# Kernel optimization log

Hardware: AMD Instinct MI355X
Metric: run time of the kernel (lower is better)

The kernel has to match this reference:

```python
import jax, jax.numpy as jnp
import numpy as np

HEIGHT, WIDTH = 480, 640
IN_CHANNEL, OUT_CHANNEL, FILTER = 6, 32, 3
B, N = 8, 16384
X_COL, Y_COL, P_COL = 1, 2, 3


def setup_inputs() -> dict:
    key = jax.random.key(0)
    k1, k2, k3, k4 = jax.random.split(key, 4)
    xytp = jax.random.uniform(k1, (B, N, 4), dtype=jnp.float32)
    features = jax.random.normal(k2, (B, N, IN_CHANNEL), dtype=jnp.float32)
    fan_in = FILTER * FILTER * (IN_CHANNEL + 2)
    W = jax.random.normal(k3, (FILTER, FILTER, IN_CHANNEL + 2, OUT_CHANNEL), dtype=jnp.float32) / jnp.sqrt(jnp.float32(fan_in))
    bias = jax.random.normal(k4, (OUT_CHANNEL,), dtype=jnp.float32) * 0.05
    return {"xytp": xytp, "features": features, "W": W, "bias": bias}


def reference(xytp, features, W, bias):
    Bc, Nc = xytp.shape[:2]
    # polarity channels: [pos, neg] concatenated with extra features -> Cin = in_channel + 2
    p = xytp[..., P_COL:P_COL + 1]
    feat = jnp.concatenate([p, 1.0 - p, features], axis=-1)  # [B, N, Cin]
    # event2image: round normalized coords to integer pixel grid (values in [0, H] / [0, W])
    yy = jnp.round(xytp[..., Y_COL] * HEIGHT).astype(jnp.int32)  # [B, N]
    xx = jnp.round(xytp[..., X_COL] * WIDTH).astype(jnp.int32)   # [B, N]
    H1, W1 = HEIGHT + 1, WIDTH + 1
    Cin = feat.shape[-1]
    bidx = jnp.broadcast_to(jnp.arange(Bc)[:, None], (Bc, Nc))
    # scn.InputLayer(mode=3): sum features at duplicate coordinates -> dense scatter-add
    grid = jnp.zeros((Bc, H1, W1, Cin), feat.dtype).at[bidx, yy, xx].add(feat)
    # SubmanifoldConvolution: inactive sites hold zero features, so a dense SAME conv
    # computes the identical gather+GEMM+scatter result at every active site.
    out_grid = jax.lax.conv_general_dilated(
        grid, W, window_strides=(1, 1), padding='SAME',
        dimension_numbers=('NHWC', 'HWIO', 'NHWC')) + bias
    # scn.OutputLayer: each input event reads the feature at its (b, y, x) site
    return out_grid[bidx, yy, xx]  # [B, N, out_channel]
```

## Files before the change

kernel.cpp:

```cpp
#include <hip/hip_runtime.h>
#include <hip/hip_bf16.h>

#define HEIGHT 480
#define WIDTH  640
#define IN_CH  6
#define CIN    8
#define COUT   32
#define BATCH  8
#define NPTS   16384
#define NPTOT  (BATCH * NPTS)
#define GH 483
#define GW 643
#define NCELLS ((size_t)BATCH * GH * GW)
#define NWORDS 77644

__device__ __forceinline__ size_t cell_idx(int b, int gy, int gx) {
    return ((size_t)b * GH + gy) * GW + gx;
}

__device__ __forceinline__ void point_cell(const float4 q, int point,
                                           int& b, int& gy, int& gx) {
    gy = (int)rintf(q.z * (float)HEIGHT) + 1;
    gx = (int)rintf(q.y * (float)WIDTH) + 1;
    b  = point >> 14;
}

__global__ void zero_masks_kernel(uint4* __restrict__ m4, int n4) {
    int i = blockIdx.x * blockDim.x + threadIdx.x;
    if (i < n4) m4[i] = make_uint4(0u, 0u, 0u, 0u);
}

__global__ void count_kernel(const float4* __restrict__ xytp,
                             unsigned int* __restrict__ occ,
                             unsigned int* __restrict__ multi) {
    int point = blockIdx.x * blockDim.x + threadIdx.x;
    if (point >= NPTOT) return;
    float4 q = xytp[point];
    int b, gy, gx;
    point_cell(q, point, b, gy, gx);
    size_t ci = cell_idx(b, gy, gx);
    unsigned int word = (unsigned int)(ci >> 5);
    unsigned int bit  = 1u << (ci & 31);
    unsigned int old = atomicOr(&occ[word], bit);
    if (old & bit) atomicOr(&multi[word], bit);
}

__global__ void prep_kernel(const unsigned int* __restrict__ multi,
                            float* __restrict__ grid) {
    int w = blockIdx.x * blockDim.x + threadIdx.x;
    if (w >= NWORDS) return;
    unsigned int m = multi[w];
    const float4 z = make_float4(0.f, 0.f, 0.f, 0.f);
    while (m) {
        int bpos = __ffs(m) - 1;
        m &= m - 1;
        size_t ci = ((size_t)w << 5) + bpos;
        float* cell = grid + (ci << 3);
        *(float4*)(cell)     = z;
        *(float4*)(cell + 4) = z;
    }
}

__global__ void write_kernel(const float4* __restrict__ xytp,
                             const float*  __restrict__ feats,
                             const unsigned int* __restrict__ multi,
                             float* __restrict__ grid) {
    int point = blockIdx.x * blockDim.x + threadIdx.x;
    if (point >= NPTOT) return;
    float4 q = xytp[point];
    int b, gy, gx;
    point_cell(q, point, b, gy, gx);
    size_t ci = cell_idx(b, gy, gx);

    const float* f = feats + (size_t)point * IN_CH;
    float v0 = q.w, v1 = 1.0f - q.w;
    float f0 = f[0], f1 = f[1], f2 = f[2], f3 = f[3], f4 = f[4], f5 = f[5];

    unsigned int word = (unsigned int)(ci >> 5);
    unsigned int bit  = 1u << (ci & 31);

    float* cell = grid + (ci << 3);
    if (!(multi[word] & bit)) {
        *(float4*)(cell)     = make_float4(v0, v1, f0, f1);
        *(float4*)(cell + 4) = make_float4(f2, f3, f4, f5);
    } else {
        unsafeAtomicAdd(cell + 0, v0);
        unsafeAtomicAdd(cell + 1, v1);
        unsafeAtomicAdd(cell + 2, f0);
        unsafeAtomicAdd(cell + 3, f1);
        unsafeAtomicAdd(cell + 4, f2);
        unsafeAtomicAdd(cell + 5, f3);
        unsafeAtomicAdd(cell + 6, f4);
        unsafeAtomicAdd(cell + 7, f5);
    }
}

__global__ void conv_gather_kernel(const float4* __restrict__ xytp,
                                   const float*  __restrict__ grid,
                                   const unsigned int* __restrict__ occ,
                                   const float*  __restrict__ W,
                                   const float*  __restrict__ bias,
                                   float* __restrict__ out) {
    int idx = blockIdx.x * blockDim.x + threadIdx.x;
    if (idx >= NPTOT) return;
    float4 q = xytp[idx];
    int b, gy, gx;
    point_cell(q, idx, b, gy, gx);
    size_t base_ci = cell_idx(b, gy - 1, gx - 1);

    float acc[COUT];
#pragma unroll
    for (int c = 0; c < COUT; ++c) acc[c] = bias[c];

#pragma unroll
    for (int ky = 0; ky < 3; ++ky) {
        size_t ci_row = base_ci + (size_t)ky * GW;
        size_t word = ci_row >> 5;
        int sh = (int)(ci_row & 31);
        unsigned int w0 = occ[word];
        unsigned int w1 = occ[word + 1];
        unsigned int bits = (unsigned int)(((((unsigned long long)w1) << 32) | w0) >> sh) & 7u;
#pragma unroll
        for (int kx = 0; kx < 3; ++kx) {
            if (bits & (1u << kx)) {
                size_t ci = ci_row + kx;
                const float* cell = grid + (ci << 3);
                float4 g0 = *(const float4*)(cell);
                float4 g1 = *(const float4*)(cell + 4);
                float gv[CIN] = {g0.x, g0.y, g0.z, g0.w, g1.x, g1.y, g1.z, g1.w};
                const float* wp = W + (ky * 3 + kx) * CIN * COUT;
#pragma unroll
                for (int ci2 = 0; ci2 < CIN; ++ci2) {
#pragma unroll
                    for (int c = 0; c < COUT; ++c) {
                        acc[c] = fmaf(gv[ci2], wp[ci2 * COUT + c], acc[c]);
                    }
                }
            }
        }
    }

    float* o = out + (size_t)idx * COUT;
#pragma unroll
    for (int c = 0; c < COUT; c += 4) {
        *(float4*)(o + c) = make_float4(acc[c], acc[c + 1], acc[c + 2], acc[c + 3]);
    }
}

extern "C" void kernel_launch(void* const* d_in, const int* in_sizes, int n_in,
                              void* d_out, int out_size, void* d_ws, size_t ws_size,
                              hipStream_t stream) {
    const float4* xytp  = (const float4*)d_in[0];
    const float*  feats = (const float*)d_in[1];
    const float*  W     = (const float*)d_in[2];
    const float*  bias  = (const float*)d_in[3];
    float* out = (float*)d_out;

    float* grid = (float*)d_ws;
    const size_t grid_bytes = NCELLS * CIN * sizeof(float);
    unsigned int* occ   = (unsigned int*)((char*)d_ws + grid_bytes);
    unsigned int* multi = occ + NWORDS;
    (void)ws_size;

    const int blk = 256;
    const int nblk_pts = (NPTOT + blk - 1) / blk;

    const int n4 = (2 * NWORDS) / 4;
    zero_masks_kernel<<<(n4 + blk - 1) / blk, blk, 0, stream>>>((uint4*)occ, n4);

    count_kernel<<<nblk_pts, blk, 0, stream>>>(xytp, occ, multi);

    prep_kernel<<<(NWORDS + blk - 1) / blk, blk, 0, stream>>>(multi, grid);

    write_kernel<<<nblk_pts, blk, 0, stream>>>(xytp, feats, multi, grid);

    conv_gather_kernel<<<nblk_pts, blk, 0, stream>>>(xytp, grid, occ, W, bias, out);
}
```

Before: 44.97 us.

## Merge prep into count kernel and split conv gather across output halves

Drops the separate prep kernel: count_kernel now zeroes a cell itself when it sees a duplicate hit, which saves one launch. The conv gather kernel runs two threads per point, each computing 16 output channels, to double parallelism and cut accumulator registers. All 9 neighbour loads are issued up front without branches (an unoccupied neighbour loads the centre cell and is masked to zero), so loads can overlap instead of being serialised by divergent branches. The cost is that grid loads and occupancy-bit work are duplicated across the two halves, and the masked FMAs are always executed.

```diff
diff --git a/kernel.cpp b/kernel.cpp
--- a/kernel.cpp
+++ b/kernel.cpp
@@ -32,7 +32,8 @@
 
 __global__ void count_kernel(const float4* __restrict__ xytp,
                              unsigned int* __restrict__ occ,
-                             unsigned int* __restrict__ multi) {
+                             unsigned int* __restrict__ multi,
+                             float* __restrict__ grid) {
     int point = blockIdx.x * blockDim.x + threadIdx.x;
     if (point >= NPTOT) return;
     float4 q = xytp[point];
@@ -42,20 +43,10 @@
     unsigned int word = (unsigned int)(ci >> 5);
     unsigned int bit  = 1u << (ci & 31);
     unsigned int old = atomicOr(&occ[word], bit);
-    if (old & bit) atomicOr(&multi[word], bit);
-}
-
-__global__ void prep_kernel(const unsigned int* __restrict__ multi,
-                            float* __restrict__ grid) {
-    int w = blockIdx.x * blockDim.x + threadIdx.x;
-    if (w >= NWORDS) return;
-    unsigned int m = multi[w];
-    const float4 z = make_float4(0.f, 0.f, 0.f, 0.f);
-    while (m) {
-        int bpos = __ffs(m) - 1;
-        m &= m - 1;
-        size_t ci = ((size_t)w << 5) + bpos;
+    if (old & bit) {
+        atomicOr(&multi[word], bit);
         float* cell = grid + (ci << 3);
+        const float4 z = make_float4(0.f, 0.f, 0.f, 0.f);
         *(float4*)(cell)     = z;
         *(float4*)(cell + 4) = z;
     }
@@ -95,54 +86,67 @@
     }
 }
 
-__global__ void conv_gather_kernel(const float4* __restrict__ xytp,
-                                   const float*  __restrict__ grid,
-                                   const unsigned int* __restrict__ occ,
-                                   const float*  __restrict__ W,
-                                   const float*  __restrict__ bias,
-                                   float* __restrict__ out) {
-    int idx = blockIdx.x * blockDim.x + threadIdx.x;
-    if (idx >= NPTOT) return;
-    float4 q = xytp[idx];
+__global__ void __launch_bounds__(256)
+conv_gather_kernel(const float4* __restrict__ xytp,
+                   const float*  __restrict__ grid,
+                   const unsigned int* __restrict__ occ,
+                   const float*  __restrict__ W,
+                   const float*  __restrict__ bias,
+                   float* __restrict__ out) {
+    int tid = blockIdx.x * blockDim.x + threadIdx.x;
+    if (tid >= NPTOT * 2) return;
+    int point = tid & (NPTOT - 1);
+    int half  = tid >> 17;
+    int cbase = half * 16;
+
+    float4 q = xytp[point];
     int b, gy, gx;
-    point_cell(q, idx, b, gy, gx);
-    size_t base_ci = cell_idx(b, gy - 1, gx - 1);
+    point_cell(q, point, b, gy, gx);
+    size_t center  = cell_idx(b, gy, gx);
+    size_t base_ci = center - GW - 1;
 
-    float acc[COUT];
-#pragma unroll
-    for (int c = 0; c < COUT; ++c) acc[c] = bias[c];
-
+    float4 g0[9], g1[9];
+    unsigned int occ9 = 0;
 #pragma unroll
     for (int ky = 0; ky < 3; ++ky) {
         size_t ci_row = base_ci + (size_t)ky * GW;
         size_t word = ci_row >> 5;
         int sh = (int)(ci_row & 31);
-        unsigned int w0 = occ[word];
-        unsigned int w1 = occ[word + 1];
-        unsigned int bits = (unsigned int)(((((unsigned long long)w1) << 32) | w0) >> sh) & 7u;
+        unsigned long long two =
+            (((unsigned long long)occ[word + 1]) << 32) | occ[word];
+        unsigned int bits = (unsigned int)(two >> sh) & 7u;
+        occ9 |= bits << (ky * 3);
 #pragma unroll
         for (int kx = 0; kx < 3; ++kx) {
-            if (bits & (1u << kx)) {
-                size_t ci = ci_row + kx;
-                const float* cell = grid + (ci << 3);
-                float4 g0 = *(const float4*)(cell);
-                float4 g1 = *(const float4*)(cell + 4);
-                float gv[CIN] = {g0.x, g0.y, g0.z, g0.w, g1.x, g1.y, g1.z, g1.w};
-                const float* wp = W + (ky * 3 + kx) * CIN * COUT;
+            size_t ci = (bits & (1u << kx)) ? (ci_row + kx) : center;
+            const float* cell = grid + (ci << 3);
+            g0[ky * 3 + kx] = *(const float4*)(cell);
+            g1[ky * 3 + kx] = *(const float4*)(cell + 4);
+        }
+    }
+
+    float acc[16];
 #pragma unroll
-                for (int ci2 = 0; ci2 < CIN; ++ci2) {
+    for (int c = 0; c < 16; ++c) acc[c] = bias[cbase + c];
+
 #pragma unroll
-                    for (int c = 0; c < COUT; ++c) {
-                        acc[c] = fmaf(gv[ci2], wp[ci2 * COUT + c], acc[c]);
-                    }
-                }
+    for (int k = 0; k < 9; ++k) {
+        float m = ((occ9 >> k) & 1u) ? 1.0f : 0.0f;
+        float gv[CIN] = {g0[k].x * m, g0[k].y * m, g0[k].z * m, g0[k].w * m,
+                         g1[k].x * m, g1[k].y * m, g1[k].z * m, g1[k].w * m};
+        const float* wp = W + k * CIN * COUT + cbase;
+#pragma unroll
+        for (int ci2 = 0; ci2 < CIN; ++ci2) {
+#pragma unroll
+            for (int c = 0; c < 16; ++c) {
+                acc[c] = fmaf(gv[ci2], wp[ci2 * COUT + c], acc[c]);
             }
         }
     }
 
-    float* o = out + (size_t)idx * COUT;
+    float* o = out + (size_t)point * COUT + cbase;
 #pragma unroll
-    for (int c = 0; c < COUT; c += 4) {
+    for (int c = 0; c < 16; c += 4) {
         *(float4*)(o + c) = make_float4(acc[c], acc[c + 1], acc[c + 2], acc[c + 3]);
     }
 }
@@ -168,11 +172,9 @@
     const int n4 = (2 * NWORDS) / 4;
     zero_masks_kernel<<<(n4 + blk - 1) / blk, blk, 0, stream>>>((uint4*)occ, n4);
 
-    count_kernel<<<nblk_pts, blk, 0, stream>>>(xytp, occ, multi);
-
-    prep_kernel<<<(NWORDS + blk - 1) / blk, blk, 0, stream>>>(multi, grid);
+    count_kernel<<<nblk_pts, blk, 0, stream>>>(xytp, occ, multi, grid);
 
     write_kernel<<<nblk_pts, blk, 0, stream>>>(xytp, feats, multi, grid);
 
-    conv_gather_kernel<<<nblk_pts, blk, 0, stream>>>(xytp, grid, occ, W, bias, out);
+    conv_gather_kernel<<<nblk_pts * 2, blk, 0, stream>>>(xytp, grid, occ, W, bias, out);
 }
```

Result: slower. 76.29 us (+69.7%).
